# Kernel optimization log

Measured on AMD Instinct MI355X. Metric: run time of the kernel, lower is better.

The kernel has to match this reference:

```python
import jax, jax.numpy as jnp
import numpy as np

D_MODEL = 256
NHEAD = 8
LEVELS = 3
POINTS = 4
DFF = 1024
HEAD_DIM = D_MODEL // NHEAD


def setup_inputs() -> dict:
    key = jax.random.key(0)
    ks = jax.random.split(key, 12)
    B = 4
    shapes = np.array([[80, 80], [40, 40], [20, 20]], dtype=np.int64)  # (H, W) per level
    sizes = shapes.prod(axis=1)
    Lq = int(sizes.sum())  # 8400
    lsi = np.concatenate([np.zeros(1, dtype=np.int64), np.cumsum(sizes)[:-1]]).astype(np.int64)

    def lin(k, fi, fo, scale=1.0):
        w = jax.random.normal(k, (fi, fo), jnp.float32)
        return w * np.float32(scale * np.sqrt(2.0 / (fi + fo)))

    return {
        'src': jax.random.normal(ks[0], (B, Lq, D_MODEL), jnp.float32),
        'reference_points': jax.random.uniform(ks[1], (B, Lq, LEVELS, 2), jnp.float32),
        'query_pos_embed': jax.random.normal(ks[2], (B, Lq, D_MODEL), jnp.float32),
        'spatial_shapes': shapes,
        'level_start_index': lsi,
        'off_w': lin(ks[3], D_MODEL, NHEAD * LEVELS * POINTS * 2, 0.1),
        'off_b': jnp.zeros((NHEAD * LEVELS * POINTS * 2,), jnp.float32),
        'aw_w': lin(ks[4], D_MODEL, NHEAD * LEVELS * POINTS),
        'aw_b': jnp.zeros((NHEAD * LEVELS * POINTS,), jnp.float32),
        'val_w': lin(ks[5], D_MODEL, D_MODEL),
        'val_b': jnp.zeros((D_MODEL,), jnp.float32),
        'out_w': lin(ks[6], D_MODEL, D_MODEL),
        'out_b': jnp.zeros((D_MODEL,), jnp.float32),
        'lin1_w': lin(ks[7], D_MODEL, DFF),
        'lin1_b': jnp.zeros((DFF,), jnp.float32),
        'lin2_w': lin(ks[8], DFF, D_MODEL),
        'lin2_b': jnp.zeros((D_MODEL,), jnp.float32),
        'ln1_g': jnp.ones((D_MODEL,), jnp.float32),
        'ln1_b': jnp.zeros((D_MODEL,), jnp.float32),
        'ln2_g': jnp.ones((D_MODEL,), jnp.float32),
        'ln2_b': jnp.zeros((D_MODEL,), jnp.float32),
    }


def layer_norm(x, g, b, eps=1e-5):
    m = x.mean(-1, keepdims=True)
    v = x.var(-1, keepdims=True)
    return (x - m) * jax.lax.rsqrt(v + eps) * g + b


def ms_deform_attn(value, shapes, lsi, loc, attn):
    # value: [B, Lv, nH, D]; loc: [B, Lq, nH, L, P, 2] in [0,1]; attn: [B, Lq, nH, L, P]
    B, Lq = loc.shape[0], loc.shape[1]
    out = jnp.zeros((B, NHEAD, Lq, HEAD_DIM), value.dtype)
    for l in range(LEVELS):
        H, W = int(shapes[l, 0]), int(shapes[l, 1])
        s = int(lsi[l])
        val = value[:, s:s + H * W].transpose(0, 2, 1, 3)  # [B, nH, HW, D]
        x = loc[:, :, :, l, :, 0] * W - 0.5  # [B, Lq, nH, P] pixel coords (align_corners=False)
        y = loc[:, :, :, l, :, 1] * H - 0.5
        x0 = jnp.floor(x)
        y0 = jnp.floor(y)
        fx = x - x0
        fy = y - y0
        x0i = x0.astype(jnp.int32)
        y0i = y0.astype(jnp.int32)
        samp = jnp.zeros((B, NHEAD, Lq, POINTS, HEAD_DIM), value.dtype)
        for dx, dy, w in ((0, 0, (1 - fx) * (1 - fy)), (1, 0, fx * (1 - fy)),
                          (0, 1, (1 - fx) * fy), (1, 1, fx * fy)):
            xi = x0i + dx
            yi = y0i + dy
            valid = (xi >= 0) & (xi < W) & (yi >= 0) & (yi < H)  # zero padding
            idx = jnp.clip(yi, 0, H - 1) * W + jnp.clip(xi, 0, W - 1)  # [B, Lq, nH, P]
            idx_t = idx.transpose(0, 2, 1, 3).reshape(B, NHEAD, Lq * POINTS)
            g = jnp.take_along_axis(val, idx_t[..., None], axis=2)
            g = g.reshape(B, NHEAD, Lq, POINTS, HEAD_DIM)
            wm = (w * valid).transpose(0, 2, 1, 3)[..., None]  # [B, nH, Lq, P, 1]
            samp = samp + g * wm
        a = attn[:, :, :, l].transpose(0, 2, 1, 3)  # [B, nH, Lq, P]
        out = out + jnp.einsum('bhqpd,bhqp->bhqd', samp, a)
    return out.transpose(0, 2, 1, 3).reshape(B, Lq, NHEAD * HEAD_DIM)


def reference(src, reference_points, query_pos_embed, spatial_shapes, level_start_index,
              off_w, off_b, aw_w, aw_b, val_w, val_b, out_w, out_b,
              lin1_w, lin1_b, lin2_w, lin2_b, ln1_g, ln1_b, ln2_g, ln2_b):
    shapes = np.asarray(spatial_shapes)
    lsi = np.asarray(level_start_index)
    B, Lq, C = src.shape
    q = src + query_pos_embed  # with_pos_embed
    value = (src @ val_w + val_b).reshape(B, Lq, NHEAD, HEAD_DIM)
    offsets = (q @ off_w + off_b).reshape(B, Lq, NHEAD, LEVELS, POINTS, 2)
    aw = (q @ aw_w + aw_b).reshape(B, Lq, NHEAD, LEVELS * POINTS)
    aw = jax.nn.softmax(aw, axis=-1).reshape(B, Lq, NHEAD, LEVELS, POINTS)
    # offset normalizer is (W, H) per level
    norm = jnp.asarray(shapes[:, ::-1].copy(), src.dtype)  # [L, 2]
    loc = reference_points[:, :, None, :, None, :] + offsets / norm[None, None, None, :, None, :]
    attn_out = ms_deform_attn(value, shapes, lsi, loc, aw) @ out_w + out_b
    h = layer_norm(src + attn_out, ln1_g, ln1_b)  # dropout1 is identity at eval
    ffn = jax.nn.gelu(h @ lin1_w + lin1_b, approximate=False) @ lin2_w + lin2_b
    return layer_norm(h + ffn, ln2_g, ln2_b)
```

## Files before the change

kernel.cpp:

```cpp
#include <hip/hip_runtime.h>

#define D_MODEL 256
#define NHEAD 8
#define HEAD_DIM 32
#define LEVELS 3
#define POINTS 4
#define DFF 1024
#define LQ 8400
#define BATCH 4
#define M_ROWS (BATCH * LQ)
#define NOFF 192
#define NAW 96

typedef __attribute__((ext_vector_type(8))) short bf16x8;
typedef __attribute__((ext_vector_type(4))) float f32x4;
#define MFMA16(a, b, c) __builtin_amdgcn_mfma_f32_16x16x32_bf16(a, b, c, 0, 0, 0)

__device__ __forceinline__ float gelu_fast(float x) {
    float u = 1.5957691216f * x * (1.f + 0.044715f * x * x);
    return x / (1.f + __expf(-u));
}

__device__ __forceinline__ unsigned short f2bf_rne(float f) {
    unsigned int u = __float_as_uint(f);
    u += 0x7fff + ((u >> 16) & 1);
    return (unsigned short)(u >> 16);
}

__device__ __forceinline__ float bf2f(unsigned short v) {
    return __uint_as_float(((unsigned)v) << 16);
}

__global__ __launch_bounds__(256) void k_wprep(
    const float* __restrict__ w1, const float* __restrict__ w2,
    const float* __restrict__ val_w, const float* __restrict__ out_w,
    const float* __restrict__ off_w, const float* __restrict__ aw_w,
    unsigned short* __restrict__ w1s, unsigned short* __restrict__ w2s,
    unsigned short* __restrict__ valws, unsigned short* __restrict__ outws,
    unsigned short* __restrict__ qws)
{
    int idx = blockIdx.x * 256 + threadIdx.x;
    int j = idx & 7, lane = (idx >> 3) & 63, rest = idx >> 9;
    int k = (lane >> 4) * 8 + j;
    int cc = lane & 15;
    {
        int nt = rest & 63, kt = rest >> 6;
        w1s[idx] = f2bf_rne(w1[(size_t)(kt * 32 + k) * DFF + nt * 16 + cc]);
    }
    {
        int nt = rest & 15, kt = rest >> 4;
        w2s[idx] = f2bf_rne(w2[(size_t)(kt * 32 + k) * D_MODEL + nt * 16 + cc]);
    }
    if (idx < 65536) {
        int nt = rest & 15, kt = rest >> 4;
        valws[idx] = f2bf_rne(val_w[(size_t)(kt * 32 + k) * D_MODEL + nt * 16 + cc]);
        outws[idx] = f2bf_rne(out_w[(size_t)(kt * 32 + k) * D_MODEL + nt * 16 + cc]);
    }
    if (idx < 73728) {
        int nt = rest % 18, kt = rest / 18;
        int col = nt * 16 + cc;
        float v = (col < NOFF) ? off_w[(size_t)(kt * 32 + k) * NOFF + col]
                               : aw_w[(size_t)(kt * 32 + k) * NAW + (col - NOFF)];
        qws[idx] = f2bf_rne(v);
    }
}

__global__ __launch_bounds__(256) void k_prep_mfma(
    const float* __restrict__ src, const float* __restrict__ qpe,
    const unsigned short* __restrict__ valws, const float* __restrict__ val_b,
    const unsigned short* __restrict__ qws, const float* __restrict__ off_b,
    const float* __restrict__ aw_b,
    unsigned short* __restrict__ valueb, float* __restrict__ offs,
    float* __restrict__ aw)
{
    __shared__ unsigned short Xs[64 * 256];
    __shared__ unsigned short Xq[64 * 256];
    float (*awl)[NAW] = (float(*)[NAW])Xs;

    const int tid = threadIdx.x;
    const int w = tid >> 6, lane = tid & 63;
    const int g = lane >> 4, c = lane & 15;
    const int r0 = blockIdx.x * 64;

    for (int i = tid; i < 64 * 32; i += 256) {
        int row = i >> 5, c8 = (i & 31) * 8;
        const float4* ps = (const float4*)(src + (size_t)(r0 + row) * D_MODEL + c8);
        const float4* pq = (const float4*)(qpe + (size_t)(r0 + row) * D_MODEL + c8);
        float4 s0 = ps[0], s1 = ps[1];
        float4 q0 = pq[0], q1 = pq[1];
        q0.x += s0.x; q0.y += s0.y; q0.z += s0.z; q0.w += s0.w;
        q1.x += s1.x; q1.y += s1.y; q1.z += s1.z; q1.w += s1.w;
        uint4 pks, pkq;
        pks.x = (unsigned)f2bf_rne(s0.x) | ((unsigned)f2bf_rne(s0.y) << 16);
        pks.y = (unsigned)f2bf_rne(s0.z) | ((unsigned)f2bf_rne(s0.w) << 16);
        pks.z = (unsigned)f2bf_rne(s1.x) | ((unsigned)f2bf_rne(s1.y) << 16);
        pks.w = (unsigned)f2bf_rne(s1.z) | ((unsigned)f2bf_rne(s1.w) << 16);
        pkq.x = (unsigned)f2bf_rne(q0.x) | ((unsigned)f2bf_rne(q0.y) << 16);
        pkq.y = (unsigned)f2bf_rne(q0.z) | ((unsigned)f2bf_rne(q0.w) << 16);
        pkq.z = (unsigned)f2bf_rne(q1.x) | ((unsigned)f2bf_rne(q1.y) << 16);
        pkq.w = (unsigned)f2bf_rne(q1.z) | ((unsigned)f2bf_rne(q1.w) << 16);
        int di = (row * 256 + c8) ^ ((row & 7) << 3);
        *(uint4*)&Xs[di] = pks;
        *(uint4*)&Xq[di] = pkq;
    }
    __syncthreads();

    const int arow = w * 16 + c;
    const int aidx0 = (arow * 256) ^ ((arow & 7) << 3);

    {
        f32x4 accv[16];
        #pragma unroll
        for (int nt = 0; nt < 16; ++nt) accv[nt] = (f32x4){0.f, 0.f, 0.f, 0.f};
        #pragma unroll
        for (int kt = 0; kt < 8; ++kt) {
            bf16x8 af = *(const bf16x8*)&Xs[aidx0 ^ (kt * 32 + g * 8)];
            #pragma unroll
            for (int nt = 0; nt < 16; ++nt) {
                bf16x8 bf = *(const bf16x8*)&valws[(size_t)((kt * 16 + nt) * 64 + lane) * 8];
                accv[nt] = MFMA16(af, bf, accv[nt]);
            }
        }
        #pragma unroll
        for (int nt = 0; nt < 16; ++nt) {
            float bias = val_b[nt * 16 + c];
            int hh = nt >> 1, dd = (nt & 1) * 16 + c;
            #pragma unroll
            for (int r = 0; r < 4; ++r) {
                int rg = r0 + w * 16 + g * 4 + r;
                int b = rg / LQ, qr = rg - b * LQ;
                valueb[(((size_t)b * NHEAD + hh) * LQ + qr) * HEAD_DIM + dd] =
                    f2bf_rne(accv[nt][r] + bias);
            }
        }
    }
    __syncthreads();

    {
        f32x4 accq[18];
        #pragma unroll
        for (int nt = 0; nt < 18; ++nt) accq[nt] = (f32x4){0.f, 0.f, 0.f, 0.f};
        #pragma unroll
        for (int kt = 0; kt < 8; ++kt) {
            bf16x8 af = *(const bf16x8*)&Xq[aidx0 ^ (kt * 32 + g * 8)];
            #pragma unroll
            for (int nt = 0; nt < 18; ++nt) {
                bf16x8 bf = *(const bf16x8*)&qws[(size_t)((kt * 18 + nt) * 64 + lane) * 8];
                accq[nt] = MFMA16(af, bf, accq[nt]);
            }
        }
        #pragma unroll
        for (int nt = 0; nt < 12; ++nt) {
            float bias = off_b[nt * 16 + c];
            #pragma unroll
            for (int r = 0; r < 4; ++r) {
                int row = w * 16 + g * 4 + r;
                offs[(size_t)(r0 + row) * NOFF + nt * 16 + c] = accq[nt][r] + bias;
            }
        }
        #pragma unroll
        for (int nt2 = 0; nt2 < 6; ++nt2) {
            float bias = aw_b[nt2 * 16 + c];
            #pragma unroll
            for (int r = 0; r < 4; ++r) {
                int row = w * 16 + g * 4 + r;
                awl[row][nt2 * 16 + c] = accq[nt2 + 12][r] + bias;
            }
        }
    }
    __syncthreads();

    for (int task = tid; task < 64 * NHEAD; task += 256) {
        int row = task >> 3, hh = task & 7;
        const float* p = &awl[row][hh * 12];
        float m = p[0];
        #pragma unroll
        for (int j = 1; j < 12; ++j) m = fmaxf(m, p[j]);
        float e[12];
        float sum = 0.f;
        #pragma unroll
        for (int j = 0; j < 12; ++j) { e[j] = __expf(p[j] - m); sum += e[j]; }
        float inv = 1.f / sum;
        float* o = &aw[(size_t)(r0 + row) * NAW + hh * 12];
        #pragma unroll
        for (int j = 0; j < 12; ++j) o[j] = e[j] * inv;
    }
}

__global__ __launch_bounds__(256) void k_sample(
    const float* __restrict__ rp, const unsigned short* __restrict__ valueb,
    const float* __restrict__ offs, const float* __restrict__ aw,
    float* __restrict__ attn)
{
    __shared__ int   s_x0[2][NAW];
    __shared__ int   s_y0[2][NAW];
    __shared__ float s_fx[2][NAW];
    __shared__ float s_fy[2][NAW];
    __shared__ float s_w[2][NAW];

    const int tid = threadIdx.x;
    const int row0 = blockIdx.x * 2;

    if (tid < 2 * NAW) {
        int rl = tid / NAW;
        int t  = tid - rl * NAW;
        int row = row0 + rl;
        const int h = t / 12, lp = t % 12, l = lp >> 2, p = lp & 3;
        const int dims[LEVELS] = {80, 40, 20};
        const int Wl = dims[l];
        float refx = rp[((size_t)row * LEVELS + l) * 2 + 0];
        float refy = rp[((size_t)row * LEVELS + l) * 2 + 1];
        size_t obase = (size_t)row * NOFF + (size_t)((h * LEVELS + l) * POINTS + p) * 2;
        float ox = offs[obase + 0];
        float oy = offs[obase + 1];
        float x = refx * (float)Wl + ox - 0.5f;
        float y = refy * (float)Wl + oy - 0.5f;
        float x0f = floorf(x), y0f = floorf(y);
        s_x0[rl][t] = (int)x0f;
        s_y0[rl][t] = (int)y0f;
        s_fx[rl][t] = x - x0f;
        s_fy[rl][t] = y - y0f;
        s_w[rl][t]  = aw[(size_t)row * NAW + t];
    }
    __syncthreads();

    const int rl = tid >> 7;
    const int hh = (tid >> 4) & 7;
    const int dp = tid & 15;
    const int row = row0 + rl;
    const int b = row / LQ;
    const unsigned short* vb =
        valueb + (((size_t)b * NHEAD + hh) * LQ) * HEAD_DIM + dp * 2;
    float accx = 0.f, accy = 0.f;

    #pragma unroll
    for (int lp = 0; lp < 12; ++lp) {
        const int l = lp >> 2;
        const int dims[LEVELS] = {80, 40, 20};
        const int lsis[LEVELS] = {0, 6400, 8000};
        const int W = dims[l], H = dims[l], s = lsis[l];
        const int t = hh * 12 + lp;
        int x0 = s_x0[rl][t], y0 = s_y0[rl][t];
        float fx = s_fx[rl][t], fy = s_fy[rl][t], w = s_w[rl][t];
        float w00 = (1.f - fx) * (1.f - fy);
        float w10 = fx * (1.f - fy);
        float w01 = (1.f - fx) * fy;
        float w11 = fx * fy;
        int x1 = x0 + 1, y1 = y0 + 1;
        bool xv0 = (x0 >= 0) && (x0 < W);
        bool xv1 = (x1 >= 0) && (x1 < W);
        bool yv0 = (y0 >= 0) && (y0 < H);
        bool yv1 = (y1 >= 0) && (y1 < H);
        unsigned u00 = 0, u10 = 0, u01 = 0, u11 = 0;
        if (xv0 && yv0) u00 = *(const unsigned*)&vb[(size_t)(s + y0 * W + x0) * HEAD_DIM];
        if (xv1 && yv0) u10 = *(const unsigned*)&vb[(size_t)(s + y0 * W + x1) * HEAD_DIM];
        if (xv0 && yv1) u01 = *(const unsigned*)&vb[(size_t)(s + y1 * W + x0) * HEAD_DIM];
        if (xv1 && yv1) u11 = *(const unsigned*)&vb[(size_t)(s + y1 * W + x1) * HEAD_DIM];
        float sx = w00 * bf2f((unsigned short)u00) + w10 * bf2f((unsigned short)u10)
                 + w01 * bf2f((unsigned short)u01) + w11 * bf2f((unsigned short)u11);
        float sy = w00 * bf2f((unsigned short)(u00 >> 16)) + w10 * bf2f((unsigned short)(u10 >> 16))
                 + w01 * bf2f((unsigned short)(u01 >> 16)) + w11 * bf2f((unsigned short)(u11 >> 16));
        accx += w * sx;
        accy += w * sy;
    }
    float2 o; o.x = accx; o.y = accy;
    *(float2*)&attn[(size_t)row * D_MODEL + hh * HEAD_DIM + dp * 2] = o;
}

__global__ __launch_bounds__(256, 2) void k_mlp(
    const float* __restrict__ attn, const float* __restrict__ src,
    const unsigned short* __restrict__ outws, const float* __restrict__ out_b,
    const float* __restrict__ ln1g, const float* __restrict__ ln1b,
    const unsigned short* __restrict__ w1s, const float* __restrict__ lin1b,
    const unsigned short* __restrict__ w2s, const float* __restrict__ lin2b,
    const float* __restrict__ ln2g, const float* __restrict__ ln2b,
    float* __restrict__ out)
{
    __shared__ unsigned short Xb[32 * 256];
    __shared__ unsigned short Y1c[2][32 * 136];
    __shared__ float psum[2][32][4];
    __shared__ float rowm[32], rowr[32];

    const int tid = threadIdx.x;
    const int w = tid >> 6, lane = tid & 63;
    const int g = lane >> 4, c = lane & 15;
    const int r0 = blockIdx.x * 32;

    for (int i = tid; i < 32 * 32; i += 256) {
        int row = i >> 5, c8 = (i & 31) * 8;
        const float4* p = (const float4*)(attn + (size_t)(r0 + row) * D_MODEL + c8);
        float4 v0 = p[0], v1 = p[1];
        uint4 pk;
        pk.x = (unsigned)f2bf_rne(v0.x) | ((unsigned)f2bf_rne(v0.y) << 16);
        pk.y = (unsigned)f2bf_rne(v0.z) | ((unsigned)f2bf_rne(v0.w) << 16);
        pk.z = (unsigned)f2bf_rne(v1.x) | ((unsigned)f2bf_rne(v1.y) << 16);
        pk.w = (unsigned)f2bf_rne(v1.z) | ((unsigned)f2bf_rne(v1.w) << 16);
        int di = (row * 256 + c8) ^ ((row & 7) << 3);
        *(uint4*)&Xb[di] = pk;
    }
    __syncthreads();

    {
        f32x4 hacc[2][4];
        #pragma unroll
        for (int m = 0; m < 2; ++m)
            #pragma unroll
            for (int n = 0; n < 4; ++n)
                hacc[m][n] = (f32x4){0.f, 0.f, 0.f, 0.f};

        #pragma unroll
        for (int half = 0; half < 2; ++half) {
            bf16x8 wfa[16];
            #pragma unroll
            for (int kt = 0; kt < 4; ++kt)
                #pragma unroll
                for (int n = 0; n < 4; ++n)
                    wfa[kt * 4 + n] = *(const bf16x8*)
                        &outws[(size_t)(((half * 4 + kt) * 16 + w * 4 + n) * 64 + lane) * 8];
            #pragma unroll
            for (int kt = 0; kt < 4; ++kt) {
                bf16x8 af[2];
                #pragma unroll
                for (int m = 0; m < 2; ++m) {
                    int row = m * 16 + c;
                    af[m] = *(const bf16x8*)
                        &Xb[(row * 256 + (half * 4 + kt) * 32 + g * 8) ^ ((row & 7) << 3)];
                }
                #pragma unroll
                for (int n = 0; n < 4; ++n)
                    #pragma unroll
                    for (int m = 0; m < 2; ++m)
                        hacc[m][n] = MFMA16(af[m], wfa[kt * 4 + n], hacc[m][n]);
            }
        }
        float ob[4], lg[4], lb[4];
        #pragma unroll
        for (int n = 0; n < 4; ++n) {
            int col = w * 64 + n * 16 + c;
            ob[n] = out_b[col]; lg[n] = ln1g[col]; lb[n] = ln1b[col];
        }
        #pragma unroll
        for (int m = 0; m < 2; ++m)
            #pragma unroll
            for (int n = 0; n < 4; ++n)
                #pragma unroll
                for (int r = 0; r < 4; ++r) {
                    int row = m * 16 + g * 4 + r;
                    int col = w * 64 + n * 16 + c;
                    hacc[m][n][r] += ob[n] + src[(size_t)(r0 + row) * D_MODEL + col];
                }
        #pragma unroll
        for (int m = 0; m < 2; ++m)
            #pragma unroll
            for (int r = 0; r < 4; ++r) {
                float s = 0.f, s2 = 0.f;
                #pragma unroll
                for (int n = 0; n < 4; ++n) {
                    float v = hacc[m][n][r];
                    s += v; s2 += v * v;
                }
                #pragma unroll
                for (int mask = 1; mask < 16; mask <<= 1) {
                    s  += __shfl_xor(s, mask);
                    s2 += __shfl_xor(s2, mask);
                }
                if (c == 0) {
                    int row = m * 16 + g * 4 + r;
                    psum[0][row][w] = s;
                    psum[1][row][w] = s2;
                }
            }
        __syncthreads();
        if (tid < 32) {
            float s  = psum[0][tid][0] + psum[0][tid][1] + psum[0][tid][2] + psum[0][tid][3];
            float s2 = psum[1][tid][0] + psum[1][tid][1] + psum[1][tid][2] + psum[1][tid][3];
            float mn = s * (1.f / D_MODEL);
            float var = s2 * (1.f / D_MODEL) - mn * mn;
            rowm[tid] = mn;
            rowr[tid] = rsqrtf(var + 1e-5f);
        }
        __syncthreads();
        #pragma unroll
        for (int m = 0; m < 2; ++m)
            #pragma unroll
            for (int n = 0; n < 4; ++n)
                #pragma unroll
                for (int r = 0; r < 4; ++r) {
                    int row = m * 16 + g * 4 + r;
                    int col = w * 64 + n * 16 + c;
                    float v = (hacc[m][n][r] - rowm[row]) * rowr[row] * lg[n] + lb[n];
                    Xb[(row * 256 + col) ^ ((row & 7) << 3)] = f2bf_rne(v);
                }
    }
    __syncthreads();

    f32x4 acc2[2][4];
    #pragma unroll
    for (int m = 0; m < 2; ++m)
        #pragma unroll
        for (int n = 0; n < 4; ++n)
            acc2[m][n] = (f32x4){0.f, 0.f, 0.f, 0.f};

    bf16x8 wf1[16];
    bf16x8 wf2[16];

    #pragma unroll
    for (int kt = 0; kt < 8; ++kt) {
        wf1[kt * 2 + 0] = *(const bf16x8*)&w1s[(size_t)((kt * 64 + w * 2 + 0) * 64 + lane) * 8];
        wf1[kt * 2 + 1] = *(const bf16x8*)&w1s[(size_t)((kt * 64 + w * 2 + 1) * 64 + lane) * 8];
    }
    {
        f32x4 acc1[2][2];
        #pragma unroll
        for (int m = 0; m < 2; ++m) {
            acc1[m][0] = (f32x4){0.f, 0.f, 0.f, 0.f};
            acc1[m][1] = (f32x4){0.f, 0.f, 0.f, 0.f};
        }
        #pragma unroll
        for (int kt = 0; kt < 8; ++kt) {
            bf16x8 af[2];
            #pragma unroll
            for (int m = 0; m < 2; ++m) {
                int row = m * 16 + c;
                af[m] = *(const bf16x8*)&Xb[(row * 256 + kt * 32 + g * 8) ^ ((row & 7) << 3)];
            }
            #pragma unroll
            for (int m = 0; m < 2; ++m) {
                acc1[m][0] = MFMA16(af[m], wf1[kt * 2 + 0], acc1[m][0]);
                acc1[m][1] = MFMA16(af[m], wf1[kt * 2 + 1], acc1[m][1]);
            }
        }
        #pragma unroll
        for (int kt2 = 0; kt2 < 4; ++kt2)
            #pragma unroll
            for (int n = 0; n < 4; ++n)
                wf2[kt2 * 4 + n] = *(const bf16x8*)
                    &w2s[(size_t)(((kt2)*16 + w * 4 + n) * 64 + lane) * 8];
        #pragma unroll
        for (int kt = 0; kt < 8; ++kt) {
            wf1[kt * 2 + 0] = *(const bf16x8*)&w1s[(size_t)((kt * 64 + 8 + w * 2 + 0) * 64 + lane) * 8];
            wf1[kt * 2 + 1] = *(const bf16x8*)&w1s[(size_t)((kt * 64 + 8 + w * 2 + 1) * 64 + lane) * 8];
        }
        float bias0 = lin1b[w * 32 + c];
        float bias1 = lin1b[w * 32 + 16 + c];
        #pragma unroll
        for (int m = 0; m < 2; ++m)
            #pragma unroll
            for (int nt = 0; nt < 2; ++nt)
                #pragma unroll
                for (int r = 0; r < 4; ++r) {
                    int row = m * 16 + g * 4 + r;
                    Y1c[0][row * 136 + w * 32 + nt * 16 + c] =
                        f2bf_rne(gelu_fast(acc1[m][nt][r] + (nt ? bias1 : bias0)));
                }
    }
    __syncthreads();

    for (int nc = 0; nc < 8; ++nc) {
        const unsigned short* yb = Y1c[nc & 1];
        #pragma unroll
        for (int kt2 = 0; kt2 < 4; ++kt2) {
            bf16x8 a2[2];
            #pragma unroll
            for (int m = 0; m < 2; ++m) {
                int row = m * 16 + c;
                a2[m] = *(const bf16x8*)&yb[row * 136 + kt2 * 32 + g * 8];
            }
            #pragma unroll
            for (int n = 0; n < 4; ++n)
                #pragma unroll
                for (int m = 0; m < 2; ++m)
                    acc2[m][n] = MFMA16(a2[m], wf2[kt2 * 4 + n], acc2[m][n]);
        }
        if (nc < 7) {
            #pragma unroll
            for (int kt2 = 0; kt2 < 4; ++kt2)
                #pragma unroll
                for (int n = 0; n < 4; ++n)
                    wf2[kt2 * 4 + n] = *(const bf16x8*)
                        &w2s[(size_t)((((nc + 1) * 4 + kt2) * 16 + w * 4 + n) * 64 + lane) * 8];
            f32x4 acc1[2][2];
            #pragma unroll
            for (int m = 0; m < 2; ++m) {
                acc1[m][0] = (f32x4){0.f, 0.f, 0.f, 0.f};
                acc1[m][1] = (f32x4){0.f, 0.f, 0.f, 0.f};
            }
            #pragma unroll
            for (int kt = 0; kt < 8; ++kt) {
                bf16x8 af[2];
                #pragma unroll
                for (int m = 0; m < 2; ++m) {
                    int row = m * 16 + c;
                    af[m] = *(const bf16x8*)&Xb[(row * 256 + kt * 32 + g * 8) ^ ((row & 7) << 3)];
                }
                #pragma unroll
                for (int m = 0; m < 2; ++m) {
                    acc1[m][0] = MFMA16(af[m], wf1[kt * 2 + 0], acc1[m][0]);
                    acc1[m][1] = MFMA16(af[m], wf1[kt * 2 + 1], acc1[m][1]);
                }
            }
            if (nc < 6) {
                const int ncc = (nc + 2) * 8;
                #pragma unroll
                for (int kt = 0; kt < 8; ++kt) {
                    wf1[kt * 2 + 0] = *(const bf16x8*)
                        &w1s[(size_t)((kt * 64 + ncc + w * 2 + 0) * 64 + lane) * 8];
                    wf1[kt * 2 + 1] = *(const bf16x8*)
                        &w1s[(size_t)((kt * 64 + ncc + w * 2 + 1) * 64 + lane) * 8];
                }
            }
            float bias0 = lin1b[(nc + 1) * 128 + w * 32 + c];
            float bias1 = lin1b[(nc + 1) * 128 + w * 32 + 16 + c];
            unsigned short* yw = Y1c[(nc + 1) & 1];
            #pragma unroll
            for (int m = 0; m < 2; ++m)
                #pragma unroll
                for (int nt = 0; nt < 2; ++nt)
                    #pragma unroll
                    for (int r = 0; r < 4; ++r) {
                        int row = m * 16 + g * 4 + r;
                        yw[row * 136 + w * 32 + nt * 16 + c] =
                            f2bf_rne(gelu_fast(acc1[m][nt][r] + (nt ? bias1 : bias0)));
                    }
        }
        __syncthreads();
    }

    float b2c[4], g2c[4], bb2c[4];
    #pragma unroll
    for (int n = 0; n < 4; ++n) {
        int col = w * 64 + n * 16 + c;
        b2c[n] = lin2b[col]; g2c[n] = ln2g[col]; bb2c[n] = ln2b[col];
    }
    #pragma unroll
    for (int m = 0; m < 2; ++m)
        #pragma unroll
        for (int n = 0; n < 4; ++n)
            #pragma unroll
            for (int r = 0; r < 4; ++r) {
                int row = m * 16 + g * 4 + r;
                int col = w * 64 + n * 16 + c;
                float hres = bf2f(Xb[(row * 256 + col) ^ ((row & 7) << 3)]);
                acc2[m][n][r] += b2c[n] + hres;
            }
    #pragma unroll
    for (int m = 0; m < 2; ++m)
        #pragma unroll
        for (int r = 0; r < 4; ++r) {
            float s = 0.f, s2 = 0.f;
            #pragma unroll
            for (int n = 0; n < 4; ++n) {
                float v = acc2[m][n][r];
                s += v; s2 += v * v;
            }
            #pragma unroll
            for (int mask = 1; mask < 16; mask <<= 1) {
                s  += __shfl_xor(s, mask);
                s2 += __shfl_xor(s2, mask);
            }
            if (c == 0) {
                int row = m * 16 + g * 4 + r;
                psum[0][row][w] = s;
                psum[1][row][w] = s2;
            }
        }
    __syncthreads();
    if (tid < 32) {
        float s  = psum[0][tid][0] + psum[0][tid][1] + psum[0][tid][2] + psum[0][tid][3];
        float s2 = psum[1][tid][0] + psum[1][tid][1] + psum[1][tid][2] + psum[1][tid][3];
        float mn = s * (1.f / D_MODEL);
        float var = s2 * (1.f / D_MODEL) - mn * mn;
        rowm[tid] = mn;
        rowr[tid] = rsqrtf(var + 1e-5f);
    }
    __syncthreads();
    #pragma unroll
    for (int m = 0; m < 2; ++m)
        #pragma unroll
        for (int n = 0; n < 4; ++n)
            #pragma unroll
            for (int r = 0; r < 4; ++r) {
                int row = m * 16 + g * 4 + r;
                int col = w * 64 + n * 16 + c;
                float v = (acc2[m][n][r] - rowm[row]) * rowr[row] * g2c[n] + bb2c[n];
                out[(size_t)(r0 + row) * D_MODEL + col] = v;
            }
}

extern "C" void kernel_launch(void* const* d_in, const int* in_sizes, int n_in,
                              void* d_out, int out_size, void* d_ws, size_t ws_size,
                              hipStream_t stream) {
    const float* src   = (const float*)d_in[0];
    const float* rp    = (const float*)d_in[1];
    const float* qpe   = (const float*)d_in[2];
    const float* off_w = (const float*)d_in[5];
    const float* off_b = (const float*)d_in[6];
    const float* aw_w  = (const float*)d_in[7];
    const float* aw_b  = (const float*)d_in[8];
    const float* val_w = (const float*)d_in[9];
    const float* val_b = (const float*)d_in[10];
    const float* out_w = (const float*)d_in[11];
    const float* out_b = (const float*)d_in[12];
    const float* w1    = (const float*)d_in[13];
    const float* b1    = (const float*)d_in[14];
    const float* w2    = (const float*)d_in[15];
    const float* b2    = (const float*)d_in[16];
    const float* ln1g  = (const float*)d_in[17];
    const float* ln1b  = (const float*)d_in[18];
    const float* ln2g  = (const float*)d_in[19];
    const float* ln2b  = (const float*)d_in[20];
    float* out = (float*)d_out;

    float* ws    = (float*)d_ws;
    float* value = ws;
    float* offs  = value + (size_t)M_ROWS * D_MODEL;
    float* aw    = offs + (size_t)M_ROWS * NOFF;
    float* attn  = aw + (size_t)M_ROWS * NAW;
    unsigned short* valueb = (unsigned short*)value;
    unsigned short* w1s   = (unsigned short*)(attn + (size_t)M_ROWS * D_MODEL);
    unsigned short* w2s   = w1s + 262144;
    unsigned short* valws = w2s + 262144;
    unsigned short* outws = valws + 65536;
    unsigned short* qws   = outws + 65536;

    k_wprep<<<1024, 256, 0, stream>>>(w1, w2, val_w, out_w, off_w, aw_w,
                                      w1s, w2s, valws, outws, qws);
    k_prep_mfma<<<M_ROWS / 64, 256, 0, stream>>>(src, qpe, valws, val_b,
                                                 qws, off_b, aw_b,
                                                 valueb, offs, aw);
    k_sample<<<M_ROWS / 2, 256, 0, stream>>>(rp, valueb, offs, aw, attn);
    k_mlp<<<M_ROWS / 32, 256, 0, stream>>>(attn, src, outws, out_b,
                                           ln1g, ln1b, w1s, b1, w2s, b2,
                                           ln2g, ln2b, out);
}
```

Before: 246.6 us.

## Store sampled attention as bf16 and prefetch weight fragments in projection GEMM

The sampling kernel now writes its attention output as packed bf16 instead of fp32, and the MLP kernel loads it directly into shared memory without converting. This halves the traffic for the 32.6k x 256 intermediate in both kernels. Separately, the projection kernel loads all B fragments for a k-step into registers before issuing the MFMAs and declares a minimum of 2 blocks per SM, to overlap global loads and raise occupancy. The larger register arrays may cause spills under the tighter launch bound. Rounding matches what k_mlp already did, so numerics should not change.

```diff
diff --git a/kernel.cpp b/kernel.cpp
--- a/kernel.cpp
+++ b/kernel.cpp
@@ -65,7 +65,7 @@
     }
 }
 
-__global__ __launch_bounds__(256) void k_prep_mfma(
+__global__ __launch_bounds__(256, 2) void k_prep_mfma(
     const float* __restrict__ src, const float* __restrict__ qpe,
     const unsigned short* __restrict__ valws, const float* __restrict__ val_b,
     const unsigned short* __restrict__ qws, const float* __restrict__ off_b,
@@ -114,12 +114,14 @@
         for (int nt = 0; nt < 16; ++nt) accv[nt] = (f32x4){0.f, 0.f, 0.f, 0.f};
         #pragma unroll
         for (int kt = 0; kt < 8; ++kt) {
+            bf16x8 wv[16];
+            #pragma unroll
+            for (int nt = 0; nt < 16; ++nt)
+                wv[nt] = *(const bf16x8*)&valws[(size_t)((kt * 16 + nt) * 64 + lane) * 8];
             bf16x8 af = *(const bf16x8*)&Xs[aidx0 ^ (kt * 32 + g * 8)];
             #pragma unroll
-            for (int nt = 0; nt < 16; ++nt) {
-                bf16x8 bf = *(const bf16x8*)&valws[(size_t)((kt * 16 + nt) * 64 + lane) * 8];
-                accv[nt] = MFMA16(af, bf, accv[nt]);
-            }
+            for (int nt = 0; nt < 16; ++nt)
+                accv[nt] = MFMA16(af, wv[nt], accv[nt]);
         }
         #pragma unroll
         for (int nt = 0; nt < 16; ++nt) {
@@ -142,12 +144,14 @@
         for (int nt = 0; nt < 18; ++nt) accq[nt] = (f32x4){0.f, 0.f, 0.f, 0.f};
         #pragma unroll
         for (int kt = 0; kt < 8; ++kt) {
+            bf16x8 wq[18];
+            #pragma unroll
+            for (int nt = 0; nt < 18; ++nt)
+                wq[nt] = *(const bf16x8*)&qws[(size_t)((kt * 18 + nt) * 64 + lane) * 8];
             bf16x8 af = *(const bf16x8*)&Xq[aidx0 ^ (kt * 32 + g * 8)];
             #pragma unroll
-            for (int nt = 0; nt < 18; ++nt) {
-                bf16x8 bf = *(const bf16x8*)&qws[(size_t)((kt * 18 + nt) * 64 + lane) * 8];
-                accq[nt] = MFMA16(af, bf, accq[nt]);
-            }
+            for (int nt = 0; nt < 18; ++nt)
+                accq[nt] = MFMA16(af, wq[nt], accq[nt]);
         }
         #pragma unroll
         for (int nt = 0; nt < 12; ++nt) {
@@ -190,7 +194,7 @@
 __global__ __launch_bounds__(256) void k_sample(
     const float* __restrict__ rp, const unsigned short* __restrict__ valueb,
     const float* __restrict__ offs, const float* __restrict__ aw,
-    float* __restrict__ attn)
+    unsigned short* __restrict__ attnb)
 {
     __shared__ int   s_x0[2][NAW];
     __shared__ int   s_y0[2][NAW];
@@ -263,12 +267,12 @@
         accx += w * sx;
         accy += w * sy;
     }
-    float2 o; o.x = accx; o.y = accy;
-    *(float2*)&attn[(size_t)row * D_MODEL + hh * HEAD_DIM + dp * 2] = o;
+    unsigned pk = (unsigned)f2bf_rne(accx) | ((unsigned)f2bf_rne(accy) << 16);
+    *(unsigned*)&attnb[(size_t)row * D_MODEL + hh * HEAD_DIM + dp * 2] = pk;
 }
 
 __global__ __launch_bounds__(256, 2) void k_mlp(
-    const float* __restrict__ attn, const float* __restrict__ src,
+    const unsigned short* __restrict__ attnb, const float* __restrict__ src,
     const unsigned short* __restrict__ outws, const float* __restrict__ out_b,
     const float* __restrict__ ln1g, const float* __restrict__ ln1b,
     const unsigned short* __restrict__ w1s, const float* __restrict__ lin1b,
@@ -288,13 +292,7 @@
 
     for (int i = tid; i < 32 * 32; i += 256) {
         int row = i >> 5, c8 = (i & 31) * 8;
-        const float4* p = (const float4*)(attn + (size_t)(r0 + row) * D_MODEL + c8);
-        float4 v0 = p[0], v1 = p[1];
-        uint4 pk;
-        pk.x = (unsigned)f2bf_rne(v0.x) | ((unsigned)f2bf_rne(v0.y) << 16);
-        pk.y = (unsigned)f2bf_rne(v0.z) | ((unsigned)f2bf_rne(v0.w) << 16);
-        pk.z = (unsigned)f2bf_rne(v1.x) | ((unsigned)f2bf_rne(v1.y) << 16);
-        pk.w = (unsigned)f2bf_rne(v1.z) | ((unsigned)f2bf_rne(v1.w) << 16);
+        uint4 pk = *(const uint4*)&attnb[(size_t)(r0 + row) * D_MODEL + c8];
         int di = (row * 256 + c8) ^ ((row & 7) << 3);
         *(uint4*)&Xb[di] = pk;
     }
@@ -617,6 +615,7 @@
     float* aw    = offs + (size_t)M_ROWS * NOFF;
     float* attn  = aw + (size_t)M_ROWS * NAW;
     unsigned short* valueb = (unsigned short*)value;
+    unsigned short* attnb  = (unsigned short*)attn;
     unsigned short* w1s   = (unsigned short*)(attn + (size_t)M_ROWS * D_MODEL);
     unsigned short* w2s   = w1s + 262144;
     unsigned short* valws = w2s + 262144;
@@ -628,8 +627,8 @@
     k_prep_mfma<<<M_ROWS / 64, 256, 0, stream>>>(src, qpe, valws, val_b,
                                                  qws, off_b, aw_b,
                                                  valueb, offs, aw);
-    k_sample<<<M_ROWS / 2, 256, 0, stream>>>(rp, valueb, offs, aw, attn);
-    k_mlp<<<M_ROWS / 32, 256, 0, stream>>>(attn, src, outws, out_b,
+    k_sample<<<M_ROWS / 2, 256, 0, stream>>>(rp, valueb, offs, aw, attnb);
+    k_mlp<<<M_ROWS / 32, 256, 0, stream>>>(attnb, src, outws, out_b,
                                            ln1g, ln1b, w1s, b1, w2s, b2,
                                            ln2g, ln2b, out);
 }
```

Measured after the change: 225.1 us. -8.7%, faster.
